# Kernel tuning notes

Measured on AMD Instinct MI355X. Metric: run time of the kernel, lower is better.

## Reference

```python
import jax, jax.numpy as jnp
import numpy as np

B, I, H, WR, UR = 4096, 512, 1024, 128, 128

def setup_inputs() -> dict:
    key = jax.random.key(0)
    ks = jax.random.split(key, 12)
    inp = {
        "x": jax.random.normal(ks[0], (B, I), jnp.float32),
        "h": jax.random.normal(ks[1], (B, H), jnp.float32),
        "c": jax.random.normal(ks[2], (B, H), jnp.float32),
        "U_x": 0.1 * jax.random.normal(ks[3], (I, WR), jnp.float32),
        "U_h": 0.1 * jax.random.normal(ks[4], (H, UR), jnp.float32),
        "V_x": 0.1 * jax.random.normal(ks[5], (4 * H, WR), jnp.float32),
        "V_h": 0.1 * jax.random.normal(ks[6], (4 * H, UR), jnp.float32),
        "b_x": 0.1 * jax.random.normal(ks[7], (4 * H,), jnp.float32),
        "b_h": 0.1 * jax.random.normal(ks[8], (4 * H,), jnp.float32),
        "dia_x": 0.1 * jax.random.normal(ks[9], (1, I), jnp.float32),
        "dia_h": 0.1 * jax.random.normal(ks[10], (1, H), jnp.float32),
    }
    return inp

def reference(x, h, c, U_x, U_h, V_x, V_h, b_x, b_h, dia_x, dia_h):
    b, i = x.shape
    hid = h.shape[1]
    # low-rank GEMMs: [B,4H]
    lowered_x = (x @ U_x) @ V_x.T
    lowered_h = (h @ U_h) @ V_h.T
    # per-gate diagonal corrections (vectorized over the 4 gates)
    V_x4 = V_x.reshape(4, hid, -1)          # [4,H,WR]
    corr_x = jnp.sum(U_x[None] * V_x4[:, :i, :], axis=-1)   # [4,I]
    vm_refined_x = x[:, None, :] * corr_x[None]              # [B,4,I]
    vm_refined_x = jnp.pad(vm_refined_x, ((0, 0), (0, 0), (0, hid - i))).reshape(b, 4 * hid)
    V_h4 = V_h.reshape(4, hid, -1)          # [4,H,UR]
    corr_h = jnp.sum(U_h[None] * V_h4, axis=-1)              # [4,H]
    vm_refined_h = (h[:, None, :] * corr_h[None]).reshape(b, 4 * hid)
    gx = lowered_x - vm_refined_x + b_x
    gh = lowered_h - vm_refined_h + b_h
    # diagonal (vector-multiplication) terms, x-part zero-padded to hidden size
    vm_x = jnp.pad(dia_x * x, ((0, 0), (0, hid - i)))        # [B,H]
    vm_h = dia_h * h                                          # [B,H]
    add = vm_x + vm_h
    xi, xf, xo, xn = jnp.split(gx, 4, axis=1)
    hi, hf, ho, hn = jnp.split(gh, 4, axis=1)
    inputgate = jax.nn.sigmoid(xi + hi + add)
    forgetgate = jax.nn.sigmoid(xf + hf + add)
    outputgate = jax.nn.sigmoid(xo + ho + add)
    newgate = jnp.tanh(xn + hn + add)
    c_next = forgetgate * c + inputgate * newgate
    h_next = outputgate * jnp.tanh(c_next)
    return (h_next, c_next)
```

## Files before the change

kernel.cpp:

```cpp
#include <hip/hip_runtime.h>

#define BB 4096
#define II 512
#define HH 1024
#define RR 128

typedef __bf16 bf16x8 __attribute__((ext_vector_type(8)));
typedef float  f32x4  __attribute__((ext_vector_type(4)));
typedef unsigned short u16x8 __attribute__((ext_vector_type(8)));
typedef unsigned short u16x4 __attribute__((ext_vector_type(4)));

__device__ __forceinline__ unsigned short f2bf(float f) {
  unsigned int u = __float_as_uint(f);
  u += 0x7fffu + ((u >> 16) & 1u);
  return (unsigned short)(u >> 16);
}
__device__ __forceinline__ float sigm(float v) { return 1.f / (1.f + __expf(-v)); }
__device__ __forceinline__ float tanh_f(float v) { return 1.f - 2.f / (1.f + __expf(2.f * v)); }


__global__ __launch_bounds__(256) void prep_kernel(
    const float* __restrict__ Ux, const float* __restrict__ Uh,
    const float* __restrict__ Vx, const float* __restrict__ Vh,
    const float* __restrict__ bx, const float* __restrict__ bh,
    unsigned short* __restrict__ VC, unsigned short* __restrict__ UTX,
    unsigned short* __restrict__ UTH, float* __restrict__ CX,
    float* __restrict__ CH, float* __restrict__ BC)
{
  int tid = blockIdx.x * 256 + threadIdx.x;
  if (tid < 131072) {
    int row = tid >> 5, kc = tid & 31, k = kc * 8;
    int jb = row >> 7, nt = row & 127, g = nt >> 5, j = jb * 32 + (nt & 31);
    int vrow = g * HH + j;
    const float* src = (k < 128) ? (Vx + vrow * RR + k) : (Vh + vrow * RR + (k - 128));
    f32x4 a = *(const f32x4*)src;
    f32x4 b = *(const f32x4*)(src + 4);
    u16x8 o;
    o[0]=f2bf(a[0]); o[1]=f2bf(a[1]); o[2]=f2bf(a[2]); o[3]=f2bf(a[3]);
    o[4]=f2bf(b[0]); o[5]=f2bf(b[1]); o[6]=f2bf(b[2]); o[7]=f2bf(b[3]);
    *(u16x8*)(VC + row * 256 + k) = o;
  } else if (tid < 139264) {
    int idx = tid - 131072;
    int n = idx & 127, k = (idx >> 7) * 8;
    u16x8 o;
    #pragma unroll
    for (int e = 0; e < 8; ++e) o[e] = f2bf(Ux[(k + e) * RR + n]);
    *(u16x8*)(UTX + n * II + k) = o;
  } else if (tid < 155648) {
    int idx = tid - 139264;
    int n = idx & 127, k = (idx >> 7) * 8;
    u16x8 o;
    #pragma unroll
    for (int e = 0; e < 8; ++e) o[e] = f2bf(Uh[(k + e) * RR + n]);
    *(u16x8*)(UTH + n * HH + k) = o;
  } else if (tid < 157696) {
    int idx = tid - 155648;
    int g = idx >> 9, i = idx & 511;
    const float* u = Ux + i * RR;
    const float* v = Vx + (g * HH + i) * RR;
    float s = 0.f;
    #pragma unroll 8
    for (int r4 = 0; r4 < 32; ++r4) {
      f32x4 uu = *(const f32x4*)(u + r4 * 4);
      f32x4 vv = *(const f32x4*)(v + r4 * 4);
      s += uu[0]*vv[0] + uu[1]*vv[1] + uu[2]*vv[2] + uu[3]*vv[3];
    }
    CX[g * II + i] = s;
  } else if (tid < 161792) {
    int idx = tid - 157696;
    int g = idx >> 10, j = idx & 1023;
    const float* u = Uh + j * RR;
    const float* v = Vh + (g * HH + j) * RR;
    float s = 0.f;
    #pragma unroll 8
    for (int r4 = 0; r4 < 32; ++r4) {
      f32x4 uu = *(const f32x4*)(u + r4 * 4);
      f32x4 vv = *(const f32x4*)(v + r4 * 4);
      s += uu[0]*vv[0] + uu[1]*vv[1] + uu[2]*vv[2] + uu[3]*vv[3];
    }
    CH[g * HH + j] = s;
  } else if (tid < 165888) {
    int n = tid - 161792;
    BC[n] = bx[n] + bh[n];
  }
}

template<int K, int NKS>
__device__ __forceinline__ void s1_core(
    const float* __restrict__ src, const unsigned short* __restrict__ Ut,
    unsigned short* __restrict__ T, float* __restrict__ Red,
    int b0, int p, int t)
{
  int l = t & 63, w = t >> 6;
  int row = l & 15, kof = (l >> 4) * 8;
  int kc0 = w * (K / 4);
  const float* ap = src + (b0 + row) * K + kc0 + kof;
  const unsigned short* bp = Ut + row * K + kc0 + kof;

  f32x4 acc[8];
  #pragma unroll
  for (int fi = 0; fi < 8; ++fi) acc[fi] = (f32x4){0.f, 0.f, 0.f, 0.f};

  #pragma unroll
  for (int ks = 0; ks < NKS; ++ks) {
    f32x4 a0 = *(const f32x4*)(ap + ks * 32);
    f32x4 a1 = *(const f32x4*)(ap + ks * 32 + 4);
    union { bf16x8 v; unsigned short u[8]; } af;
    af.u[0]=f2bf(a0[0]); af.u[1]=f2bf(a0[1]); af.u[2]=f2bf(a0[2]); af.u[3]=f2bf(a0[3]);
    af.u[4]=f2bf(a1[0]); af.u[5]=f2bf(a1[1]); af.u[6]=f2bf(a1[2]); af.u[7]=f2bf(a1[3]);
    #pragma unroll
    for (int fi = 0; fi < 8; ++fi) {
      bf16x8 bf = *(const bf16x8*)(bp + fi * 16 * K + ks * 32);
      acc[fi] = __builtin_amdgcn_mfma_f32_16x16x32_bf16(af.v, bf, acc[fi], 0, 0, 0);
    }
  }

  #pragma unroll
  for (int fi = 0; fi < 8; ++fi) {
    int n = fi * 16 + row;
    #pragma unroll
    for (int reg = 0; reg < 4; ++reg) {
      int m = (l >> 4) * 4 + reg;
      Red[(w * 16 + m) * 132 + n] = acc[fi][reg];
    }
  }
  __syncthreads();

  #pragma unroll
  for (int it = 0; it < 2; ++it) {
    int q = it * 256 + t;
    int m = q >> 5, c4 = (q & 31) * 4;
    f32x4 s0 = *(const f32x4*)(Red + (0 * 16 + m) * 132 + c4);
    f32x4 s1 = *(const f32x4*)(Red + (1 * 16 + m) * 132 + c4);
    f32x4 s2 = *(const f32x4*)(Red + (2 * 16 + m) * 132 + c4);
    f32x4 s3 = *(const f32x4*)(Red + (3 * 16 + m) * 132 + c4);
    f32x4 s = s0 + s1 + s2 + s3;
    u16x4 o;
    o[0]=f2bf(s[0]); o[1]=f2bf(s[1]); o[2]=f2bf(s[2]); o[3]=f2bf(s[3]);
    *(u16x4*)(T + (b0 + m) * 256 + p * 128 + c4) = o;
  }
}

__global__ __launch_bounds__(256) void stage1_kernel(
    const float* __restrict__ x, const float* __restrict__ h,
    const unsigned short* __restrict__ UTX, const unsigned short* __restrict__ UTH,
    unsigned short* __restrict__ T)
{
  __shared__ alignas(16) float Red[4 * 16 * 132];
  int t = threadIdx.x;
  int mb = blockIdx.x & 255;
  if (blockIdx.x < 256) s1_core<II, II / 128>(x, UTX, T, Red, mb * 16, 0, t);
  else                  s1_core<HH, HH / 128>(h, UTH, T, Red, mb * 16, 1, t);
}

__global__ __launch_bounds__(512) void stage2_kernel(
    const unsigned short* __restrict__ T, const unsigned short* __restrict__ VC,
    const float* __restrict__ CX, const float* __restrict__ CH, const float* __restrict__ BC,
    const float* __restrict__ x, const float* __restrict__ h, const float* __restrict__ c,
    const float* __restrict__ dx, const float* __restrict__ dh,
    float* __restrict__ out)
{
  __shared__ alignas(16) unsigned short Vs[128 * 264];
  int t = threadIdx.x, l = t & 63, w = t >> 6;
  int jb = blockIdx.x >> 5, mb = blockIdx.x & 31;
  int b0 = mb * 128, j0 = jb * 32;

  #pragma unroll
  for (int i = 0; i < 8; ++i) {
    int f = i * 512 + t;
    int r = f >> 5, kc = (f & 31) * 8;
    *(u16x8*)(Vs + r * 264 + kc) = *(const u16x8*)(VC + (jb * 128 + r) * 256 + kc);
  }
  __syncthreads();

  int row = l & 15, koff = (l >> 4) * 8;
  const unsigned short* ap = T + (b0 + w * 16 + row) * 256 + koff;

  f32x4 acc[8];
  #pragma unroll
  for (int fi = 0; fi < 8; ++fi) acc[fi] = (f32x4){0.f, 0.f, 0.f, 0.f};

  #pragma unroll
  for (int ks = 0; ks < 8; ++ks) {
    bf16x8 a = *(const bf16x8*)(ap + ks * 32);
    #pragma unroll
    for (int fi = 0; fi < 8; ++fi) {
      bf16x8 b = *(const bf16x8*)(Vs + (fi * 16 + row) * 264 + ks * 32 + koff);
      acc[fi] = __builtin_amdgcn_mfma_f32_16x16x32_bf16(a, b, acc[fi], 0, 0, 0);
    }
  }

  #pragma unroll
  for (int reg = 0; reg < 4; ++reg) {
    int b = b0 + w * 16 + (l >> 4) * 4 + reg;
    #pragma unroll
    for (int hl = 0; hl < 2; ++hl) {
      int j = j0 + hl * 16 + (l & 15);
      float hv = h[b * HH + j];
      float cv = c[b * HH + j];
      float addv = dh[j] * hv;
      float pre[4];
      #pragma unroll
      for (int g = 0; g < 4; ++g) pre[g] = acc[g * 2 + hl][reg];
      if (j0 < II) {
        float xv = x[b * II + j];
        addv += dx[j] * xv;
        #pragma unroll
        for (int g = 0; g < 4; ++g) pre[g] -= xv * CX[g * II + j];
      }
      #pragma unroll
      for (int g = 0; g < 4; ++g) pre[g] += BC[g * HH + j] + addv - hv * CH[g * HH + j];
      float ig = sigm(pre[0]);
      float fg = sigm(pre[1]);
      float og = sigm(pre[2]);
      float ng = tanh_f(pre[3]);
      float cn = fg * cv + ig * ng;
      float hn = og * tanh_f(cn);
      out[b * HH + j] = hn;
      out[BB * HH + b * HH + j] = cn;
    }
  }
}

extern "C" void kernel_launch(void* const* d_in, const int* in_sizes, int n_in,
                              void* d_out, int out_size, void* d_ws, size_t ws_size,
                              hipStream_t stream) {
  const float* x  = (const float*)d_in[0];
  const float* h  = (const float*)d_in[1];
  const float* c  = (const float*)d_in[2];
  const float* Ux = (const float*)d_in[3];
  const float* Uh = (const float*)d_in[4];
  const float* Vx = (const float*)d_in[5];
  const float* Vh = (const float*)d_in[6];
  const float* bx = (const float*)d_in[7];
  const float* bh = (const float*)d_in[8];
  const float* dx = (const float*)d_in[9];
  const float* dh = (const float*)d_in[10];
  char* ws = (char*)d_ws;
  unsigned short* T   = (unsigned short*)(ws + 0);
  unsigned short* VC  = (unsigned short*)(ws + 2097152);
  unsigned short* UTX = (unsigned short*)(ws + 4194304);
  unsigned short* UTH = (unsigned short*)(ws + 4325376);
  float* CX = (float*)(ws + 4587520);
  float* CH = (float*)(ws + 4595712);
  float* BC = (float*)(ws + 4612096);
  float* out = (float*)d_out;

  prep_kernel<<<648, 256, 0, stream>>>(Ux, Uh, Vx, Vh, bx, bh, VC, UTX, UTH, CX, CH, BC);
  stage1_kernel<<<512, 256, 0, stream>>>(x, h, UTX, UTH, T);
  stage2_kernel<<<1024, 512, 0, stream>>>(T, VC, CX, CH, BC, x, h, c, dx, dh, out);
}
```

Baseline: 59.83 us.

## Keep V operand in registers and drop LDS staging in stage2 GEMM

Stage2 now gives each wave its own 8 hidden columns across all four gates. The packed V fragments are loaded once into registers, so the LDS buffer and block barrier are gone. Each wave loops over 8 batch sub-tiles and uses a lane shuffle to gather all four gate values for a column into one lane. Per-column constants are hoisted out of the loop, and blocks are remapped so each XCD covers contiguous column blocks. The cost is high register pressure from 16 persistent bf16x8 fragments, plus repeated loads of the T tile across waves.

Measured after the change: 99.37 us. 66.1% more time.

```diff
diff --git a/kernel.cpp b/kernel.cpp
--- a/kernel.cpp
+++ b/kernel.cpp
@@ -30,7 +30,11 @@
   int tid = blockIdx.x * 256 + threadIdx.x;
   if (tid < 131072) {
     int row = tid >> 5, kc = tid & 31, k = kc * 8;
-    int jb = row >> 7, nt = row & 127, g = nt >> 5, j = jb * 32 + (nt & 31);
+    int jb = row >> 8;
+    int t8 = row & 255;
+    int w = t8 >> 5, f = (t8 >> 4) & 1, cc = t8 & 15;
+    int g = f * 2 + (cc >> 3);
+    int j = jb * 64 + w * 8 + (cc & 7);
     int vrow = g * HH + j;
     const float* src = (k < 128) ? (Vx + vrow * RR + k) : (Vh + vrow * RR + (k - 128));
     f32x4 a = *(const f32x4*)src;
@@ -153,71 +157,89 @@
   else                  s1_core<HH, HH / 128>(h, UTH, T, Red, mb * 16, 1, t);
 }
 
-__global__ __launch_bounds__(512) void stage2_kernel(
+__global__ __launch_bounds__(512, 3) void stage2_kernel(
     const unsigned short* __restrict__ T, const unsigned short* __restrict__ VC,
     const float* __restrict__ CX, const float* __restrict__ CH, const float* __restrict__ BC,
     const float* __restrict__ x, const float* __restrict__ h, const float* __restrict__ c,
     const float* __restrict__ dx, const float* __restrict__ dh,
     float* __restrict__ out)
 {
-  __shared__ alignas(16) unsigned short Vs[128 * 264];
   int t = threadIdx.x, l = t & 63, w = t >> 6;
-  int jb = blockIdx.x >> 5, mb = blockIdx.x & 31;
-  int b0 = mb * 128, j0 = jb * 32;
-
-  #pragma unroll
-  for (int i = 0; i < 8; ++i) {
-    int f = i * 512 + t;
-    int r = f >> 5, kc = (f & 31) * 8;
-    *(u16x8*)(Vs + r * 264 + kc) = *(const u16x8*)(VC + (jb * 128 + r) * 256 + kc);
-  }
-  __syncthreads();
-
-  int row = l & 15, koff = (l >> 4) * 8;
-  const unsigned short* ap = T + (b0 + w * 16 + row) * 256 + koff;
-
-  f32x4 acc[8];
-  #pragma unroll
-  for (int fi = 0; fi < 8; ++fi) acc[fi] = (f32x4){0.f, 0.f, 0.f, 0.f};
-
+  int xcd = blockIdx.x & 7, idx = blockIdx.x >> 3;
+  int jb = xcd * 2 + (idx >> 5);
+  int mb = idx & 31;
+  int b0 = mb * 128, j0 = jb * 64;
+  int row = l & 15, hi = l >> 4;
+  int koff = hi * 8;
+  int ch = (l >> 3) & 1;
+  int jv = j0 + w * 8 + (l & 7);
+  bool has_x = (j0 < II);
+
+  const unsigned short* vp = VC + (jb * 256 + w * 32 + row) * 256 + koff;
+  bf16x8 bf0[8], bf1[8];
   #pragma unroll
   for (int ks = 0; ks < 8; ++ks) {
-    bf16x8 a = *(const bf16x8*)(ap + ks * 32);
-    #pragma unroll
-    for (int fi = 0; fi < 8; ++fi) {
-      bf16x8 b = *(const bf16x8*)(Vs + (fi * 16 + row) * 264 + ks * 32 + koff);
-      acc[fi] = __builtin_amdgcn_mfma_f32_16x16x32_bf16(a, b, acc[fi], 0, 0, 0);
-    }
-  }
-
-  #pragma unroll
-  for (int reg = 0; reg < 4; ++reg) {
-    int b = b0 + w * 16 + (l >> 4) * 4 + reg;
-    #pragma unroll
-    for (int hl = 0; hl < 2; ++hl) {
-      int j = j0 + hl * 16 + (l & 15);
-      float hv = h[b * HH + j];
-      float cv = c[b * HH + j];
-      float addv = dh[j] * hv;
-      float pre[4];
-      #pragma unroll
-      for (int g = 0; g < 4; ++g) pre[g] = acc[g * 2 + hl][reg];
-      if (j0 < II) {
-        float xv = x[b * II + j];
-        addv += dx[j] * xv;
-        #pragma unroll
-        for (int g = 0; g < 4; ++g) pre[g] -= xv * CX[g * II + j];
+    bf0[ks] = *(const bf16x8*)(vp + ks * 32);
+    bf1[ks] = *(const bf16x8*)(vp + 16 * 256 + ks * 32);
+  }
+
+  float dhv = dh[jv];
+  float dxv = has_x ? dx[jv] : 0.f;
+  float cxv0 = has_x ? CX[0 * II + jv] : 0.f;
+  float cxv1 = has_x ? CX[1 * II + jv] : 0.f;
+  float cxv2 = has_x ? CX[2 * II + jv] : 0.f;
+  float cxv3 = has_x ? CX[3 * II + jv] : 0.f;
+  float chv0 = CH[0 * HH + jv], chv1 = CH[1 * HH + jv];
+  float chv2 = CH[2 * HH + jv], chv3 = CH[3 * HH + jv];
+  float bcv0 = BC[0 * HH + jv], bcv1 = BC[1 * HH + jv];
+  float bcv2 = BC[2 * HH + jv], bcv3 = BC[3 * HH + jv];
+
+  const unsigned short* ap0 = T + (b0 + row) * 256 + koff;
+
+  #pragma unroll 2
+  for (int ms = 0; ms < 8; ++ms) {
+    const unsigned short* ap = ap0 + ms * 16 * 256;
+    f32x4 acc0 = (f32x4){0.f, 0.f, 0.f, 0.f};
+    f32x4 acc1 = (f32x4){0.f, 0.f, 0.f, 0.f};
+    #pragma unroll
+    for (int ks = 0; ks < 8; ++ks) {
+      bf16x8 a = *(const bf16x8*)(ap + ks * 32);
+      acc0 = __builtin_amdgcn_mfma_f32_16x16x32_bf16(a, bf0[ks], acc0, 0, 0, 0);
+      acc1 = __builtin_amdgcn_mfma_f32_16x16x32_bf16(a, bf1[ks], acc1, 0, 0, 0);
+    }
+    #pragma unroll
+    for (int rr = 0; rr < 2; ++rr) {
+      float keep0 = ch ? acc0[2 + rr] : acc0[rr];
+      float send0 = ch ? acc0[rr] : acc0[2 + rr];
+      float keep1 = ch ? acc1[2 + rr] : acc1[rr];
+      float send1 = ch ? acc1[rr] : acc1[2 + rr];
+      float recv0 = __shfl_xor(send0, 8);
+      float recv1 = __shfl_xor(send1, 8);
+      float p0 = ch ? recv0 : keep0;
+      float p1 = ch ? keep0 : recv0;
+      float p2 = ch ? recv1 : keep1;
+      float p3 = ch ? keep1 : recv1;
+      int b = b0 + ms * 16 + hi * 4 + ch * 2 + rr;
+      float hv = h[b * HH + jv];
+      float cv = c[b * HH + jv];
+      float addv = dhv * hv;
+      if (has_x) {
+        float xv = x[b * II + jv];
+        addv += dxv * xv;
+        p0 -= xv * cxv0; p1 -= xv * cxv1; p2 -= xv * cxv2; p3 -= xv * cxv3;
       }
-      #pragma unroll
-      for (int g = 0; g < 4; ++g) pre[g] += BC[g * HH + j] + addv - hv * CH[g * HH + j];
-      float ig = sigm(pre[0]);
-      float fg = sigm(pre[1]);
-      float og = sigm(pre[2]);
-      float ng = tanh_f(pre[3]);
+      p0 += bcv0 + addv - hv * chv0;
+      p1 += bcv1 + addv - hv * chv1;
+      p2 += bcv2 + addv - hv * chv2;
+      p3 += bcv3 + addv - hv * chv3;
+      float ig = sigm(p0);
+      float fg = sigm(p1);
+      float og = sigm(p2);
+      float ng = tanh_f(p3);
       float cn = fg * cv + ig * ng;
       float hn = og * tanh_f(cn);
-      out[b * HH + j] = hn;
-      out[BB * HH + b * HH + j] = cn;
+      out[b * HH + jv] = hn;
+      out[BB * HH + b * HH + jv] = cn;
     }
   }
 }
@@ -248,5 +270,5 @@
 
   prep_kernel<<<648, 256, 0, stream>>>(Ux, Uh, Vx, Vh, bx, bh, VC, UTX, UTH, CX, CH, BC);
   stage1_kernel<<<512, 256, 0, stream>>>(x, h, UTX, UTH, T);
-  stage2_kernel<<<1024, 512, 0, stream>>>(T, VC, CX, CH, BC, x, h, c, dx, dh, out);
-}
+  stage2_kernel<<<512, 512, 0, stream>>>(T, VC, CX, CH, BC, x, h, c, dx, dh, out);
+}
```
